# Performance work log

Hardware: AMD Instinct MI355X
Metric: run time of the kernel (lower is better)

Reference implementation:

```python
import jax, jax.numpy as jnp
import numpy as np


def conv3d(x, w, b=None):
    # x: (N,C,D,H,W), w: (O,I,3,3,3), stride 1, padding 1 == SAME
    y = jax.lax.conv_general_dilated(x, w, (1, 1, 1), 'SAME',
                                     dimension_numbers=('NCDHW', 'OIDHW', 'NCDHW'))
    if b is not None:
        y = y + b[None, :, None, None, None]
    return y


def grid_sample_3d(vol, gx, gy, gz):
    # vol: (B,D,H,W); gx/gy/gz: normalized coords in [-1,1], shape (B,D,H,W)
    # trilinear, zeros padding, align_corners=True (old torch default)
    B, D, H, W = vol.shape
    ix = (gx + 1.0) * 0.5 * (W - 1)
    iy = (gy + 1.0) * 0.5 * (H - 1)
    iz = (gz + 1.0) * 0.5 * (D - 1)
    x0f, y0f, z0f = jnp.floor(ix), jnp.floor(iy), jnp.floor(iz)
    tx, ty, tz = ix - x0f, iy - y0f, iz - z0f
    x0 = x0f.astype(jnp.int32)
    y0 = y0f.astype(jnp.int32)
    z0 = z0f.astype(jnp.int32)
    vol_flat = vol.reshape(B, D * H * W)
    out = jnp.zeros_like(vol)
    for dz in (0, 1):
        for dy in (0, 1):
            for dx in (0, 1):
                xc, yc, zc = x0 + dx, y0 + dy, z0 + dz
                w = ((tx if dx else 1.0 - tx) * (ty if dy else 1.0 - ty)
                     * (tz if dz else 1.0 - tz))
                inb = ((xc >= 0) & (xc < W) & (yc >= 0) & (yc < H)
                       & (zc >= 0) & (zc < D))
                idx = ((jnp.clip(zc, 0, D - 1) * H + jnp.clip(yc, 0, H - 1)) * W
                       + jnp.clip(xc, 0, W - 1))
                val = jnp.take_along_axis(vol_flat, idx.reshape(B, -1), axis=1)
                val = val.reshape(B, D, H, W) * inb.astype(vol.dtype)
                out = out + w * val
    return out


def setup_inputs() -> dict:
    key = jax.random.key(0)
    k1, k2, k3, k4 = jax.random.split(key, 4)
    B, C, Cout, S = 2, 32, 64, 64
    x = jax.random.normal(k1, (B, C, S, S, S), dtype=jnp.float32)
    w_off = jax.random.normal(k2, (3 * C, C, 3, 3, 3), dtype=jnp.float32) * 0.0005
    w_reg = jax.random.normal(k3, (Cout, C, 3, 3, 3), dtype=jnp.float32) * 0.05
    b_reg = jax.random.normal(k4, (Cout,), dtype=jnp.float32) * 0.05
    return {"x": x, "w_off": w_off, "w_reg": w_reg, "b_reg": b_reg}


def reference(x, w_off, w_reg, b_reg):
    B, C, D, H, W = x.shape
    offset = conv3d(x, w_off)  # (B, 3C, D, H, W)
    off_w, off_h, _ = jnp.split(offset, 3, axis=1)
    # NOTE: original code has offset_d = offset_h (faithful bug)
    off_d = off_h
    off_w = off_w.reshape(B * C, D, H, W)
    off_h = off_h.reshape(B * C, D, H, W)
    off_d = off_d.reshape(B * C, D, H, W)
    # np.meshgrid default 'xy' indexing: shapes (H, W, D) -> requires D==H==W
    gw, gh, gd = np.meshgrid(np.linspace(-1, 1, W), np.linspace(-1, 1, H),
                             np.linspace(-1, 1, D))
    grid_w = jnp.asarray(gw, dtype=x.dtype)
    grid_h = jnp.asarray(gh, dtype=x.dtype)
    grid_d = jnp.asarray(gd, dtype=x.dtype)
    off_w = off_w + grid_w
    off_h = off_h + grid_h
    off_d = off_d + grid_d
    vol = x.reshape(B * C, D, H, W)
    # torch grid stack order: (offset_h, offset_w, offset_d) -> (x, y, z)
    sampled = grid_sample_3d(vol, off_h, off_w, off_d)
    sampled = sampled.reshape(B, C, D, H, W)
    return conv3d(sampled, w_reg, b_reg)
```

## Files before the change

kernel.cpp:

```cpp
#include <hip/hip_runtime.h>
#include <cstddef>

#define S 64
#define VOL (64*64*64)
#define CIN 32

typedef __attribute__((ext_vector_type(8))) short bf16x8;
typedef __attribute__((ext_vector_type(4))) float floatx4;

struct __attribute__((packed, aligned(4))) fpair { float x, y; };

__device__ __forceinline__ unsigned short f2bf(float f) {
    union { float f; unsigned u; } v; v.f = f;
    unsigned r = v.u + 0x7fffu + ((v.u >> 16) & 1u);
    return (unsigned short)(r >> 16);
}
__device__ __forceinline__ float bf2f(unsigned short h) {
    union { unsigned u; float f; } v; v.u = ((unsigned)h) << 16;
    return v.f;
}
__device__ __forceinline__ int iclamp(int v, int lo, int hi) {
    return v < lo ? lo : (v > hi ? hi : v);
}

__device__ __forceinline__ void gload_lds16(const void* g, void* l) {
    __builtin_amdgcn_global_load_lds(
        (const __attribute__((address_space(1))) void*)g,
        (__attribute__((address_space(3))) void*)l, 16, 0, 0);
}

__global__ void prep_w_kernel(const float* __restrict__ w_off,
                              const float* __restrict__ w_reg,
                              unsigned short* __restrict__ wt1,
                              unsigned short* __restrict__ wt2) {
    int i = blockIdx.x * 256 + threadIdx.x;
    if (i >= 27 * 64 * 32) return;
    int ci = i & 31;
    int co = (i >> 5) & 63;
    int tap = i >> 11;
    wt1[i] = f2bf(w_off[(co * 32 + ci) * 27 + tap]);
    wt2[i] = f2bf(w_reg[(co * 32 + ci) * 27 + tap]);
}

__global__ __launch_bounds__(256)
void prepack_kernel(const float* __restrict__ x, uint4* __restrict__ xb4) {
    __shared__ uint4 pbuf[1024];
    const int t = threadIdx.x;
    const unsigned id0 = blockIdx.x * 256;
    const unsigned id  = id0 + t;
    const int b   = id >> 18;
    const int pos = id & (VOL - 1);
    const float* sp = x + (size_t)b * 32 * VOL + pos;
    float v[32];
#pragma unroll
    for (int c = 0; c < 32; ++c) v[c] = sp[(size_t)c * VOL];
#pragma unroll
    for (int i = 0; i < 4; ++i) {
        uint4 pk;
        pk.x = (unsigned)f2bf(v[i*8+0]) | ((unsigned)f2bf(v[i*8+1]) << 16);
        pk.y = (unsigned)f2bf(v[i*8+2]) | ((unsigned)f2bf(v[i*8+3]) << 16);
        pk.z = (unsigned)f2bf(v[i*8+4]) | ((unsigned)f2bf(v[i*8+5]) << 16);
        pk.w = (unsigned)f2bf(v[i*8+6]) | ((unsigned)f2bf(v[i*8+7]) << 16);
        pbuf[t * 4 + (i ^ (t & 3))] = pk;
    }
    __syncthreads();
#pragma unroll
    for (int i = 0; i < 4; ++i) {
        const int g  = i * 256 + t;
        const int ch = g & 3;
        const int lw = g >> 2;
        xb4[(size_t)id0 * 4 + g] = pbuf[lw * 4 + (ch ^ (lw & 3))];
    }
}

template <bool WRITE_OFF>
__global__ __launch_bounds__(256, 2)
void conv_mfma_kernel(const unsigned short* __restrict__ src,
                      const unsigned short* __restrict__ wt,
                      const float* __restrict__ bias,
                      void* __restrict__ dstv) {
    __shared__ unsigned short lds[16 * 64 * 32];

    const int d0 = blockIdx.x * 2;
    const int h0 = blockIdx.y * 2;
    const int b  = blockIdx.z;
    const int t  = threadIdx.x;
    const int lane = t & 63;
    const int wv   = t >> 6;

    const int sl = lane >> 2;
    const int js = (lane & 3) ^ ((lane >> 3) & 3);
    const char* sbase = (const char*)src + (size_t)b * VOL * 64;
#pragma unroll
    for (int rr2 = 0; rr2 < 4; ++rr2) {
        const int rowi = (wv << 2) + rr2;
        const int z = d0 - 1 + (rowi >> 2);
        const int y = h0 - 1 + (rowi & 3);
        char* ldsrow = (char*)lds + (rowi << 12);
        if (((unsigned)z < 64u) && ((unsigned)y < 64u)) {
            const char* gb = sbase + ((size_t)(z * 4096 + y * 64)) * 64
                           + (sl << 6) + (js << 4);
#pragma unroll
            for (int k = 0; k < 4; ++k)
                gload_lds16(gb + (k << 10), ldsrow + (k << 10));
        } else {
            const uint4 z4 = make_uint4(0, 0, 0, 0);
#pragma unroll
            for (int k = 0; k < 4; ++k)
                *(uint4*)(ldsrow + (k << 10) + (lane << 4)) = z4;
        }
    }

    const int r    = lane & 15;
    const int q    = lane >> 4;
    const int dd   = wv >> 1;
    const int hh   = wv & 1;

    int P[4][3];
#pragma unroll
    for (int nt = 0; nt < 4; ++nt)
#pragma unroll
        for (int kw = 0; kw < 3; ++kw) {
            const int s  = nt * 16 + r + kw - 1;
            const int sc = s & 63;
            P[nt][kw] = (sc << 6) + ((q ^ ((sc >> 1) & 3)) << 4);
        }

    floatx4 acc[4][4];
#pragma unroll
    for (int mt = 0; mt < 4; ++mt)
#pragma unroll
        for (int nt = 0; nt < 4; ++nt)
#pragma unroll
            for (int rg = 0; rg < 4; ++rg) acc[mt][nt][rg] = 0.f;

    asm volatile("s_waitcnt lgkmcnt(0)" ::: "memory");
    if (wv < 3) asm volatile("s_waitcnt vmcnt(0)" ::: "memory");
    __builtin_amdgcn_s_barrier();
    __builtin_amdgcn_sched_barrier(0);

    const bf16x8 z8 = {0, 0, 0, 0, 0, 0, 0, 0};

#pragma unroll
    for (int tap = 0; tap < 27; ++tap) {
        if (tap == 18) {
            if (wv == 3) asm volatile("s_waitcnt vmcnt(0)" ::: "memory");
            __builtin_amdgcn_s_barrier();
            __builtin_amdgcn_sched_barrier(0);
        }
        const int kd = tap / 9;
        const int kh = (tap % 9) / 3;
        const int kw = tap % 3;
        const int rowb = ((((dd + kd) << 2) + hh + kh) << 12);

        bf16x8 afr[4];
#pragma unroll
        for (int mt = 0; mt < 4; ++mt)
            afr[mt] = *(const bf16x8*)&wt[tap * 2048 + (mt * 16 + r) * 32 + q * 8];

        bf16x8 bfr[4];
#pragma unroll
        for (int nt = 0; nt < 4; ++nt)
            bfr[nt] = *(const bf16x8*)((const char*)lds + rowb + P[nt][kw]);

        if (kw == 0) { if (r == 0)  bfr[0] = z8; }
        if (kw == 2) { if (r == 15) bfr[3] = z8; }

#pragma unroll
        for (int mt = 0; mt < 4; ++mt)
#pragma unroll
            for (int nt = 0; nt < 4; ++nt)
                acc[mt][nt] = __builtin_amdgcn_mfma_f32_16x16x32_bf16(
                                  afr[mt], bfr[nt], acc[mt][nt], 0, 0, 0);
    }

    const int dw = (d0 + dd) * 4096 + (h0 + hh) * 64;
    if (WRITE_OFF) {
        unsigned* dst = (unsigned*)dstv + (size_t)b * VOL * 32;
#pragma unroll
        for (int mt = 0; mt < 2; ++mt) {
#pragma unroll
            for (int nt = 0; nt < 4; ++nt) {
                const int pos = dw + nt * 16 + r;
                uint4 pk;
                pk.x = (unsigned)f2bf(acc[mt][nt][0]) | ((unsigned)f2bf(acc[mt+2][nt][0]) << 16);
                pk.y = (unsigned)f2bf(acc[mt][nt][1]) | ((unsigned)f2bf(acc[mt+2][nt][1]) << 16);
                pk.z = (unsigned)f2bf(acc[mt][nt][2]) | ((unsigned)f2bf(acc[mt+2][nt][2]) << 16);
                pk.w = (unsigned)f2bf(acc[mt][nt][3]) | ((unsigned)f2bf(acc[mt+2][nt][3]) << 16);
                *(uint4*)(dst + (size_t)pos * 32 + mt * 16 + q * 4) = pk;
            }
        }
    } else {
#pragma unroll
        for (int mt = 0; mt < 4; ++mt) {
#pragma unroll
            for (int nt = 0; nt < 4; ++nt) {
#pragma unroll
                for (int rg = 0; rg < 4; ++rg) {
                    const int co  = mt * 16 + q * 4 + rg;
                    const int pos = dw + nt * 16 + r;
                    ((float*)dstv)[((size_t)(b * 64 + co)) * VOL + pos]
                        = acc[mt][nt][rg] + bias[co];
                }
            }
        }
    }
}

__global__ __launch_bounds__(256, 8)
void gather_kernel(const float* __restrict__ x,
                   const uint4* __restrict__ off4,
                   uint4* __restrict__ samp4) {
    const int t = threadIdx.x;
    const unsigned gid = blockIdx.x;
    const int b   = gid >> 10;
    const int j   = gid & 1023;
    const int wt4 = j & 3;
    const int dt  = (j >> 2) & 3;
    const int h   = j >> 4;
    const int d_i = t & 15;
    const int w_i = t >> 4;
    const int d = dt * 16 + d_i;
    const int w = wt4 * 16 + w_i;
    const int p = d * 4096 + h * 64 + w;

    const uint4* op = off4 + ((size_t)b * VOL + p) * 8;
    uint4* sp       = samp4 + ((size_t)b * VOL + p) * 4;
    const float* xb_ = x + (size_t)b * 32 * VOL;
    const float fd = (float)d, fh = (float)h, fw = (float)w;

#pragma unroll 1
    for (int g = 0; g < 4; ++g) {
        const uint4 oA = op[g * 2 + 0];
        const uint4 oB = op[g * 2 + 1];
        const unsigned oarr[8] = {oA.x, oA.y, oA.z, oA.w, oB.x, oB.y, oB.z, oB.w};
        float outv[8];
#pragma unroll
        for (int ce = 0; ce < 8; ++ce) {
            const int c = g * 8 + ce;
            const unsigned ow = oarr[ce];
            const float offw = bf2f((unsigned short)(ow & 0xffffu));
            const float offh = bf2f((unsigned short)(ow >> 16));
            const float* vol = xb_ + (size_t)c * VOL;

            const float ix = offh * 31.5f + fd;
            const float iy = offw * 31.5f + fh;
            const float iz = offh * 31.5f + fw;

            const float x0f = floorf(ix), y0f = floorf(iy), z0f = floorf(iz);
            const float tx = ix - x0f, ty = iy - y0f, tz = iz - z0f;
            const int ix0 = (int)x0f, iy0 = (int)y0f, iz0 = (int)z0f;

            const int bx0 = iclamp(ix0, 0, 62);
            const bool sel = (ix0 == bx0);
            const float w0x = ((unsigned)ix0 < 64u)       ? (1.f - tx) : 0.f;
            const float w1x = ((unsigned)(ix0 + 1) < 64u) ? tx         : 0.f;

            float out = 0.f;
#pragma unroll
            for (int dz = 0; dz < 2; ++dz) {
                const int zc = iz0 + dz;
                const bool zok = ((unsigned)zc < 64u);
                const int zcc = iclamp(zc, 0, 63);
                const float wz = dz ? tz : 1.f - tz;
#pragma unroll
                for (int dy = 0; dy < 2; ++dy) {
                    const int yc = iy0 + dy;
                    const bool yok = ((unsigned)yc < 64u);
                    const int ycc = iclamp(yc, 0, 63);
                    const float wzy = (zok && yok) ? wz * (dy ? ty : 1.f - ty) : 0.f;

                    const fpair vp = *(const fpair*)&vol[(zcc * 64 + ycc) * 64 + bx0];
                    const float v0 = sel ? vp.x : vp.y;
                    const float v1 = sel ? vp.y : vp.x;
                    out += wzy * (w0x * v0 + w1x * v1);
                }
            }
            outv[ce] = out;
        }
        uint4 pk;
        pk.x = (unsigned)f2bf(outv[0]) | ((unsigned)f2bf(outv[1]) << 16);
        pk.y = (unsigned)f2bf(outv[2]) | ((unsigned)f2bf(outv[3]) << 16);
        pk.z = (unsigned)f2bf(outv[4]) | ((unsigned)f2bf(outv[5]) << 16);
        pk.w = (unsigned)f2bf(outv[6]) | ((unsigned)f2bf(outv[7]) << 16);
        sp[g] = pk;
    }
}

extern "C" void kernel_launch(void* const* d_in, const int* in_sizes, int n_in,
                              void* d_out, int out_size, void* d_ws, size_t ws_size,
                              hipStream_t stream) {
    (void)in_sizes; (void)n_in; (void)out_size; (void)ws_size;
    const float* x     = (const float*)d_in[0];
    const float* w_off = (const float*)d_in[1];
    const float* w_reg = (const float*)d_in[2];
    const float* b_reg = (const float*)d_in[3];
    float* out = (float*)d_out;

    unsigned* off32 = (unsigned*)d_ws;
    unsigned* buf   = off32 + (size_t)2 * VOL * 32;
    unsigned short* wt1 = (unsigned short*)(buf + (size_t)2 * VOL * 16);
    unsigned short* wt2 = wt1 + 27 * 64 * 32;

    prep_w_kernel<<<216, 256, 0, stream>>>(w_off, w_reg, wt1, wt2);
    prepack_kernel<<<2048, 256, 0, stream>>>(x, (uint4*)buf);

    dim3 cgrid(32, 32, 2);
    conv_mfma_kernel<true><<<cgrid, 256, 0, stream>>>(
        (const unsigned short*)buf, wt1, nullptr, (void*)off32);

    gather_kernel<<<2048, 256, 0, stream>>>(x, (const uint4*)off32, (uint4*)buf);

    conv_mfma_kernel<false><<<cgrid, 256, 0, stream>>>(
        (const unsigned short*)buf, wt2, b_reg, (void*)out);
}
```

Baseline: 441.8 us.

## Fuse bf16 prepack into first conv and simplify conv2 load barrier

```diff
diff --git a/kernel.cpp b/kernel.cpp
--- a/kernel.cpp
+++ b/kernel.cpp
@@ -27,6 +27,11 @@
     __builtin_amdgcn_global_load_lds(
         (const __attribute__((address_space(1))) void*)g,
         (__attribute__((address_space(3))) void*)l, 16, 0, 0);
+}
+
+__device__ __forceinline__ void load4bf(const float* p, unsigned short* o) {
+    const float4 v = *(const float4*)p;
+    o[0] = f2bf(v.x); o[1] = f2bf(v.y); o[2] = f2bf(v.z); o[3] = f2bf(v.w);
 }
 
 __global__ void prep_w_kernel(const float* __restrict__ w_off,
@@ -42,43 +47,126 @@
     wt2[i] = f2bf(w_reg[(co * 32 + ci) * 27 + tap]);
 }
 
-__global__ __launch_bounds__(256)
-void prepack_kernel(const float* __restrict__ x, uint4* __restrict__ xb4) {
-    __shared__ uint4 pbuf[1024];
-    const int t = threadIdx.x;
-    const unsigned id0 = blockIdx.x * 256;
-    const unsigned id  = id0 + t;
-    const int b   = id >> 18;
-    const int pos = id & (VOL - 1);
-    const float* sp = x + (size_t)b * 32 * VOL + pos;
-    float v[32];
-#pragma unroll
-    for (int c = 0; c < 32; ++c) v[c] = sp[(size_t)c * VOL];
-#pragma unroll
-    for (int i = 0; i < 4; ++i) {
-        uint4 pk;
-        pk.x = (unsigned)f2bf(v[i*8+0]) | ((unsigned)f2bf(v[i*8+1]) << 16);
-        pk.y = (unsigned)f2bf(v[i*8+2]) | ((unsigned)f2bf(v[i*8+3]) << 16);
-        pk.z = (unsigned)f2bf(v[i*8+4]) | ((unsigned)f2bf(v[i*8+5]) << 16);
-        pk.w = (unsigned)f2bf(v[i*8+6]) | ((unsigned)f2bf(v[i*8+7]) << 16);
-        pbuf[t * 4 + (i ^ (t & 3))] = pk;
+__global__ __launch_bounds__(256, 2)
+void conv1_kernel(const float* __restrict__ src,
+                  const unsigned short* __restrict__ wt,
+                  unsigned* __restrict__ dst32) {
+    __shared__ unsigned short lds[16 * 64 * 32];
+
+    const int d0 = blockIdx.x * 2;
+    const int h0 = blockIdx.y * 2;
+    const int b  = blockIdx.z;
+    const int t  = threadIdx.x;
+
+    const float* sb = src + (size_t)b * CIN * VOL;
+
+    const int w0 = (t & 15) << 2;
+    const int c0 = (t >> 4) << 1;
+    const int jj = c0 >> 3;
+    const int cb = (c0 & 7) << 1;
+    const int sw01 = (w0 >> 1) & 3;
+    const int sw23 = ((w0 >> 1) + 1) & 3;
+
+#pragma unroll
+    for (int rr = 0; rr < 16; ++rr) {
+        const int z = d0 - 1 + (rr >> 2);
+        const int y = h0 - 1 + (rr & 3);
+        unsigned pk0 = 0, pk1 = 0, pk2 = 0, pk3 = 0;
+        if (((unsigned)z < 64u) && ((unsigned)y < 64u)) {
+            const float* p0 = sb + (size_t)c0 * VOL + (z * 64 + y) * 64 + w0;
+            unsigned short va[4], vb[4];
+            load4bf(p0, va);
+            load4bf(p0 + VOL, vb);
+            pk0 = (unsigned)va[0] | ((unsigned)vb[0] << 16);
+            pk1 = (unsigned)va[1] | ((unsigned)vb[1] << 16);
+            pk2 = (unsigned)va[2] | ((unsigned)vb[2] << 16);
+            pk3 = (unsigned)va[3] | ((unsigned)vb[3] << 16);
+        }
+        char* rbase = (char*)lds + (rr << 12) + cb;
+        *(unsigned*)(rbase + ((w0 + 0) << 6) + ((jj ^ sw01) << 4)) = pk0;
+        *(unsigned*)(rbase + ((w0 + 1) << 6) + ((jj ^ sw01) << 4)) = pk1;
+        *(unsigned*)(rbase + ((w0 + 2) << 6) + ((jj ^ sw23) << 4)) = pk2;
+        *(unsigned*)(rbase + ((w0 + 3) << 6) + ((jj ^ sw23) << 4)) = pk3;
     }
     __syncthreads();
-#pragma unroll
-    for (int i = 0; i < 4; ++i) {
-        const int g  = i * 256 + t;
-        const int ch = g & 3;
-        const int lw = g >> 2;
-        xb4[(size_t)id0 * 4 + g] = pbuf[lw * 4 + (ch ^ (lw & 3))];
-    }
-}
-
-template <bool WRITE_OFF>
+
+    const int lane = t & 63;
+    const int wv   = t >> 6;
+    const int r    = lane & 15;
+    const int q    = lane >> 4;
+    const int dd   = wv >> 1;
+    const int hh   = wv & 1;
+
+    int P[4][3];
+#pragma unroll
+    for (int nt = 0; nt < 4; ++nt)
+#pragma unroll
+        for (int kw = 0; kw < 3; ++kw) {
+            const int s  = nt * 16 + r + kw - 1;
+            const int sc = s & 63;
+            P[nt][kw] = (sc << 6) + ((q ^ ((sc >> 1) & 3)) << 4);
+        }
+
+    floatx4 acc[4][4];
+#pragma unroll
+    for (int mt = 0; mt < 4; ++mt)
+#pragma unroll
+        for (int nt = 0; nt < 4; ++nt)
+#pragma unroll
+            for (int rg = 0; rg < 4; ++rg) acc[mt][nt][rg] = 0.f;
+
+    const bf16x8 z8 = {0, 0, 0, 0, 0, 0, 0, 0};
+
+#pragma unroll
+    for (int tap = 0; tap < 27; ++tap) {
+        const int kd = tap / 9;
+        const int kh = (tap % 9) / 3;
+        const int kw = tap % 3;
+        const int rowb = ((((dd + kd) << 2) + hh + kh) << 12);
+
+        bf16x8 afr[4];
+#pragma unroll
+        for (int mt = 0; mt < 4; ++mt)
+            afr[mt] = *(const bf16x8*)&wt[tap * 2048 + (mt * 16 + r) * 32 + q * 8];
+
+        bf16x8 bfr[4];
+#pragma unroll
+        for (int nt = 0; nt < 4; ++nt)
+            bfr[nt] = *(const bf16x8*)((const char*)lds + rowb + P[nt][kw]);
+
+        if (kw == 0) { if (r == 0)  bfr[0] = z8; }
+        if (kw == 2) { if (r == 15) bfr[3] = z8; }
+
+#pragma unroll
+        for (int mt = 0; mt < 4; ++mt)
+#pragma unroll
+            for (int nt = 0; nt < 4; ++nt)
+                acc[mt][nt] = __builtin_amdgcn_mfma_f32_16x16x32_bf16(
+                                  afr[mt], bfr[nt], acc[mt][nt], 0, 0, 0);
+    }
+
+    const int dw = (d0 + dd) * 4096 + (h0 + hh) * 64;
+    unsigned* dst = dst32 + (size_t)b * VOL * 32;
+#pragma unroll
+    for (int mt = 0; mt < 2; ++mt) {
+#pragma unroll
+        for (int nt = 0; nt < 4; ++nt) {
+            const int pos = dw + nt * 16 + r;
+            uint4 pk;
+            pk.x = (unsigned)f2bf(acc[mt][nt][0]) | ((unsigned)f2bf(acc[mt+2][nt][0]) << 16);
+            pk.y = (unsigned)f2bf(acc[mt][nt][1]) | ((unsigned)f2bf(acc[mt+2][nt][1]) << 16);
+            pk.z = (unsigned)f2bf(acc[mt][nt][2]) | ((unsigned)f2bf(acc[mt+2][nt][2]) << 16);
+            pk.w = (unsigned)f2bf(acc[mt][nt][3]) | ((unsigned)f2bf(acc[mt+2][nt][3]) << 16);
+            *(uint4*)(dst + (size_t)pos * 32 + mt * 16 + q * 4) = pk;
+        }
+    }
+}
+
 __global__ __launch_bounds__(256, 2)
-void conv_mfma_kernel(const unsigned short* __restrict__ src,
-                      const unsigned short* __restrict__ wt,
-                      const float* __restrict__ bias,
-                      void* __restrict__ dstv) {
+void conv2_kernel(const unsigned short* __restrict__ src,
+                  const unsigned short* __restrict__ wt,
+                  const float* __restrict__ bias,
+                  float* __restrict__ dstf) {
     __shared__ unsigned short lds[16 * 64 * 32];
 
     const int d0 = blockIdx.x * 2;
@@ -110,6 +198,7 @@
                 *(uint4*)(ldsrow + (k << 10) + (lane << 4)) = z4;
         }
     }
+    __syncthreads();
 
     const int r    = lane & 15;
     const int q    = lane >> 4;
@@ -134,20 +223,10 @@
 #pragma unroll
             for (int rg = 0; rg < 4; ++rg) acc[mt][nt][rg] = 0.f;
 
-    asm volatile("s_waitcnt lgkmcnt(0)" ::: "memory");
-    if (wv < 3) asm volatile("s_waitcnt vmcnt(0)" ::: "memory");
-    __builtin_amdgcn_s_barrier();
-    __builtin_amdgcn_sched_barrier(0);
-
     const bf16x8 z8 = {0, 0, 0, 0, 0, 0, 0, 0};
 
 #pragma unroll
     for (int tap = 0; tap < 27; ++tap) {
-        if (tap == 18) {
-            if (wv == 3) asm volatile("s_waitcnt vmcnt(0)" ::: "memory");
-            __builtin_amdgcn_s_barrier();
-            __builtin_amdgcn_sched_barrier(0);
-        }
         const int kd = tap / 9;
         const int kh = (tap % 9) / 3;
         const int kw = tap % 3;
@@ -175,33 +254,15 @@
     }
 
     const int dw = (d0 + dd) * 4096 + (h0 + hh) * 64;
-    if (WRITE_OFF) {
-        unsigned* dst = (unsigned*)dstv + (size_t)b * VOL * 32;
-#pragma unroll
-        for (int mt = 0; mt < 2; ++mt) {
-#pragma unroll
-            for (int nt = 0; nt < 4; ++nt) {
+#pragma unroll
+    for (int mt = 0; mt < 4; ++mt) {
+#pragma unroll
+        for (int nt = 0; nt < 4; ++nt) {
+#pragma unroll
+            for (int rg = 0; rg < 4; ++rg) {
+                const int co  = mt * 16 + q * 4 + rg;
                 const int pos = dw + nt * 16 + r;
-                uint4 pk;
-                pk.x = (unsigned)f2bf(acc[mt][nt][0]) | ((unsigned)f2bf(acc[mt+2][nt][0]) << 16);
-                pk.y = (unsigned)f2bf(acc[mt][nt][1]) | ((unsigned)f2bf(acc[mt+2][nt][1]) << 16);
-                pk.z = (unsigned)f2bf(acc[mt][nt][2]) | ((unsigned)f2bf(acc[mt+2][nt][2]) << 16);
-                pk.w = (unsigned)f2bf(acc[mt][nt][3]) | ((unsigned)f2bf(acc[mt+2][nt][3]) << 16);
-                *(uint4*)(dst + (size_t)pos * 32 + mt * 16 + q * 4) = pk;
-            }
-        }
-    } else {
-#pragma unroll
-        for (int mt = 0; mt < 4; ++mt) {
-#pragma unroll
-            for (int nt = 0; nt < 4; ++nt) {
-#pragma unroll
-                for (int rg = 0; rg < 4; ++rg) {
-                    const int co  = mt * 16 + q * 4 + rg;
-                    const int pos = dw + nt * 16 + r;
-                    ((float*)dstv)[((size_t)(b * 64 + co)) * VOL + pos]
-                        = acc[mt][nt][rg] + bias[co];
-                }
+                dstf[((size_t)(b * 64 + co)) * VOL + pos] = acc[mt][nt][rg] + bias[co];
             }
         }
     }
@@ -298,19 +359,17 @@
     float* out = (float*)d_out;
 
     unsigned* off32 = (unsigned*)d_ws;
-    unsigned* buf   = off32 + (size_t)2 * VOL * 32;
-    unsigned short* wt1 = (unsigned short*)(buf + (size_t)2 * VOL * 16);
+    unsigned* sampled = off32 + (size_t)2 * VOL * 32;
+    unsigned short* wt1 = (unsigned short*)(sampled + (size_t)2 * VOL * 16);
     unsigned short* wt2 = wt1 + 27 * 64 * 32;
 
     prep_w_kernel<<<216, 256, 0, stream>>>(w_off, w_reg, wt1, wt2);
-    prepack_kernel<<<2048, 256, 0, stream>>>(x, (uint4*)buf);
 
     dim3 cgrid(32, 32, 2);
-    conv_mfma_kernel<true><<<cgrid, 256, 0, stream>>>(
-        (const unsigned short*)buf, wt1, nullptr, (void*)off32);
-
-    gather_kernel<<<2048, 256, 0, stream>>>(x, (const uint4*)off32, (uint4*)buf);
-
-    conv_mfma_kernel<false><<<cgrid, 256, 0, stream>>>(
-        (const unsigned short*)buf, wt2, b_reg, (void*)out);
-}
+    conv1_kernel<<<cgrid, 256, 0, stream>>>(x, wt1, off32);
+
+    gather_kernel<<<2048, 256, 0, stream>>>(x, (const uint4*)off32, (uint4*)sampled);
+
+    conv2_kernel<<<cgrid, 256, 0, stream>>>(
+        (const unsigned short*)sampled, wt2, b_reg, out);
+}
```

Measured after the change: 442.4 us. Within noise of the previous version (+0.1%).
